# Kernel tuning notes

Hardware: AMD Instinct MI355X
Metric: run time of the kernel (lower is better)

Reference implementation:

```python
import jax, jax.numpy as jnp
import numpy as np

RANK = 16
ALPHA = 32.0
SCALING = ALPHA / RANK  # 2.0
IN_F = 2048
OUT_F = 2048


def setup_inputs() -> dict:
    key = jax.random.key(0)
    ks = jax.random.split(key, 6)
    bs, seq = 8, 2048
    n_splits, n_skills = 4, 8
    x = jax.random.normal(ks[0], (bs, seq, IN_F), dtype=jnp.float32)
    weights = jax.random.uniform(ks[1], (bs, n_splits, n_skills), dtype=jnp.float32)
    W = jax.random.normal(ks[2], (OUT_F, IN_F), dtype=jnp.float32) * 0.02
    bias = jax.random.normal(ks[3], (OUT_F,), dtype=jnp.float32) * 0.02
    lora_a = jax.random.normal(ks[4], (n_splits, n_skills, IN_F // n_splits, RANK), dtype=jnp.float32) * 0.02
    lora_b = jax.random.normal(ks[5], (n_splits, n_skills, RANK, OUT_F // n_splits), dtype=jnp.float32) * 0.02
    return {"x": x, "weights": weights, "W": W, "bias": bias, "lora_a": lora_a, "lora_b": lora_b}


def reference(x, weights, W, bias, lora_a, lora_b):
    bs = x.shape[0]
    # base linear layer
    layer_out = jnp.einsum('bti,oi->bto', x, W) + bias
    # skill-weighted mixing of per-split LoRA factors (soft routing)
    A = jnp.einsum('bqs,qsdr->bqdr', weights, lora_a)  # [bs, q, in/q, r]
    B = jnp.einsum('bqs,qsrd->bqrd', weights, lora_b)  # [bs, q, r, out/q]
    A = A.reshape(bs, IN_F, RANK)                      # [bs, in, r]
    B = jnp.transpose(B, (0, 2, 1, 3)).reshape(bs, RANK, OUT_F)  # [bs, r, out]
    # per-sample batched low-rank matmul + scaled residual add
    adapter = jnp.einsum('bti,bir->btr', x, A)
    adapter = jnp.einsum('btr,bro->bto', adapter, B) * SCALING
    return layer_out + adapter
```

## Files before the change

### kernel.cpp

```cpp
#include <hip/hip_runtime.h>


typedef __attribute__((ext_vector_type(8))) short short8;
typedef __attribute__((ext_vector_type(4))) float f32x4;

#define INF   2048
#define OUTF  2048
#define RANK  16
#define BM    128
#define BN    128
#define BK    32

__device__ __forceinline__ unsigned short bf16rne(float f) {
    unsigned int u = __float_as_uint(f);
    unsigned int r = u + 0x7FFFu + ((u >> 16) & 1u);
    return (unsigned short)(r >> 16);
}

__device__ __forceinline__ void gload_lds16(const void* g, void* l) {
    __builtin_amdgcn_global_load_lds(
        (const __attribute__((address_space(1))) unsigned int*)g,
        (__attribute__((address_space(3))) unsigned int*)l, 16, 0, 0);
}

__global__ __launch_bounds__(256) void k_wbf16(const float4* __restrict__ W,
                                               ushort4* __restrict__ o) {
    int g = blockIdx.x * 256 + threadIdx.x;
    float4 f = W[g];
    o[g] = make_ushort4(bf16rne(f.x), bf16rne(f.y), bf16rne(f.z), bf16rne(f.w));
}

__global__ __launch_bounds__(256) void k_mix(const float* __restrict__ wts,
                                             const float* __restrict__ la,
                                             const float* __restrict__ lb,
                                             float* __restrict__ Amix,
                                             float* __restrict__ Bmix) {
    int gid = blockIdx.x * 256 + threadIdx.x;
    int b = gid >> 11, i = gid & 2047;
    int q = i >> 9, d = i & 511;
    float w[8];
#pragma unroll
    for (int s = 0; s < 8; ++s) w[s] = wts[(b * 4 + q) * 8 + s];

    float accA[16];
#pragma unroll
    for (int r = 0; r < 16; ++r) accA[r] = 0.f;
#pragma unroll
    for (int s = 0; s < 8; ++s) {
        const float4* pa = (const float4*)(la + (((q * 8 + s) * 512 + d) << 4));
        float4 a0 = pa[0], a1 = pa[1], a2 = pa[2], a3 = pa[3];
        float wv = w[s];
        accA[0]  += wv * a0.x; accA[1]  += wv * a0.y; accA[2]  += wv * a0.z; accA[3]  += wv * a0.w;
        accA[4]  += wv * a1.x; accA[5]  += wv * a1.y; accA[6]  += wv * a1.z; accA[7]  += wv * a1.w;
        accA[8]  += wv * a2.x; accA[9]  += wv * a2.y; accA[10] += wv * a2.z; accA[11] += wv * a2.w;
        accA[12] += wv * a3.x; accA[13] += wv * a3.y; accA[14] += wv * a3.z; accA[15] += wv * a3.w;
    }
    float4* pA = (float4*)(Amix + ((size_t)gid << 4));
    pA[0] = make_float4(accA[0],  accA[1],  accA[2],  accA[3]);
    pA[1] = make_float4(accA[4],  accA[5],  accA[6],  accA[7]);
    pA[2] = make_float4(accA[8],  accA[9],  accA[10], accA[11]);
    pA[3] = make_float4(accA[12], accA[13], accA[14], accA[15]);

    float accB[16];
#pragma unroll
    for (int r = 0; r < 16; ++r) accB[r] = 0.f;
#pragma unroll
    for (int s = 0; s < 8; ++s) {
        float wv = w[s];
#pragma unroll
        for (int r = 0; r < 16; ++r)
            accB[r] += wv * lb[((q * 8 + s) * 16 + r) * 512 + d];
    }
#pragma unroll
    for (int r = 0; r < 16; ++r)
        Bmix[((size_t)(b * 16 + r) << 11) + i] = 2.0f * accB[r];
}

__global__ __launch_bounds__(256) void k_xa(const float* __restrict__ x,
                                            const float* __restrict__ Amix,
                                            float* __restrict__ T) {
    int row = blockIdx.x * 4 + (threadIdx.x >> 6);
    int lane = threadIdx.x & 63;
    int b = row >> 11;
    const float* xr = x + (size_t)row * INF;
    const float4* A4 = (const float4*)(Amix + ((size_t)b << 15));

    float acc[16];
#pragma unroll
    for (int r = 0; r < 16; ++r) acc[r] = 0.f;
    for (int k = lane; k < INF; k += 64) {
        float xv = xr[k];
        float4 a0 = A4[k * 4 + 0], a1 = A4[k * 4 + 1], a2 = A4[k * 4 + 2], a3 = A4[k * 4 + 3];
        acc[0]  += xv * a0.x; acc[1]  += xv * a0.y; acc[2]  += xv * a0.z; acc[3]  += xv * a0.w;
        acc[4]  += xv * a1.x; acc[5]  += xv * a1.y; acc[6]  += xv * a1.z; acc[7]  += xv * a1.w;
        acc[8]  += xv * a2.x; acc[9]  += xv * a2.y; acc[10] += xv * a2.z; acc[11] += xv * a2.w;
        acc[12] += xv * a3.x; acc[13] += xv * a3.y; acc[14] += xv * a3.z; acc[15] += xv * a3.w;
    }
#pragma unroll
    for (int off = 1; off < 64; off <<= 1) {
#pragma unroll
        for (int r = 0; r < 16; ++r) acc[r] += __shfl_xor(acc[r], off);
    }
    int r = lane & 15;
    float a0 = (r & 1) ? acc[1]  : acc[0];
    float a1 = (r & 1) ? acc[3]  : acc[2];
    float a2 = (r & 1) ? acc[5]  : acc[4];
    float a3 = (r & 1) ? acc[7]  : acc[6];
    float a4 = (r & 1) ? acc[9]  : acc[8];
    float a5 = (r & 1) ? acc[11] : acc[10];
    float a6 = (r & 1) ? acc[13] : acc[12];
    float a7 = (r & 1) ? acc[15] : acc[14];
    float b0 = (r & 2) ? a1 : a0;
    float b1 = (r & 2) ? a3 : a2;
    float b2 = (r & 2) ? a5 : a4;
    float b3 = (r & 2) ? a7 : a6;
    float c0 = (r & 4) ? b1 : b0;
    float c1 = (r & 4) ? b3 : b2;
    float v  = (r & 8) ? c1 : c0;
    if (lane < 16) T[((size_t)row << 4) + lane] = v;
}

__global__ __launch_bounds__(256)
void k_gemm(const float* __restrict__ x,
            const unsigned short* __restrict__ Wbf,
            const float* __restrict__ bias,
            const float* __restrict__ T,
            const float* __restrict__ Bmix,
            float* __restrict__ out) {
    __shared__ __align__(16) char smem[16384];
    unsigned short* ldsA = (unsigned short*)smem;
    unsigned short* ldsB = (unsigned short*)(smem + 8192);

    const int tid = threadIdx.x;
    const int wid = tid >> 6;
    const int lane = tid & 63;

    int swz = ((blockIdx.x & 7) << 8) | (blockIdx.x >> 3);
    const int m0 = (swz >> 4) << 7;
    const int n0 = (swz & 15) << 7;
    const int b  = m0 >> 11;

    const int wm = (wid >> 1) << 6;
    const int wn = (wid & 1) << 6;

    f32x4 acc[4][4];
#pragma unroll
    for (int i = 0; i < 4; ++i)
#pragma unroll
        for (int j = 0; j < 4; ++j) acc[i][j] = (f32x4){0.f, 0.f, 0.f, 0.f};

    const int ar = tid >> 3;
    const int ac = (tid & 7) << 2;
    const float* xbase = x + (size_t)(m0 + ar) * INF + ac;

    for (int kt = 0; kt < 64; ++kt) {
        const int k0 = kt << 5;
        __syncthreads();

#pragma unroll
        for (int c = 0; c < 2; ++c) {
            int rr = (wid << 5) + (c << 4);
            int srow = n0 + rr + (lane >> 2);
            int scol = k0 + ((lane & 3) << 3);
            gload_lds16(Wbf + (size_t)srow * INF + scol, &ldsB[rr * BK]);
        }
#pragma unroll
        for (int j = 0; j < 4; ++j) {
            float4 f = *(const float4*)(xbase + (size_t)(j * 32) * INF + k0);
            int rw = (ar + j * 32) * BK + ac;
            *(ushort4*)&ldsA[rw] =
                make_ushort4(bf16rne(f.x), bf16rne(f.y), bf16rne(f.z), bf16rne(f.w));
        }
        __syncthreads();

        short8 av[4], bv[4];
        const int fr = lane & 15;
        const int fs = (lane >> 4) << 3;
#pragma unroll
        for (int mf = 0; mf < 4; ++mf)
            av[mf] = *(const short8*)&ldsA[(wm + mf * 16 + fr) * BK + fs];
#pragma unroll
        for (int nf = 0; nf < 4; ++nf)
            bv[nf] = *(const short8*)&ldsB[(wn + nf * 16 + fr) * BK + fs];
#pragma unroll
        for (int mf = 0; mf < 4; ++mf)
#pragma unroll
            for (int nf = 0; nf < 4; ++nf)
                acc[mf][nf] = __builtin_amdgcn_mfma_f32_16x16x32_bf16(av[mf], bv[nf], acc[mf][nf], 0, 0, 0);
    }

    __syncthreads();
    float* ldsT  = (float*)smem;
    float* ldsB2 = (float*)(smem + 8192);
    {
        int row = tid >> 1, half = tid & 1;
        const float* Tp = T + (((size_t)(m0 + row)) << 4) + half * 8;
        float4 v0 = *(const float4*)Tp;
        float4 v1 = *(const float4*)(Tp + 4);
        int rb = half * 8;
        ldsT[(rb + 0) * 128 + row] = v0.x;
        ldsT[(rb + 1) * 128 + row] = v0.y;
        ldsT[(rb + 2) * 128 + row] = v0.z;
        ldsT[(rb + 3) * 128 + row] = v0.w;
        ldsT[(rb + 4) * 128 + row] = v1.x;
        ldsT[(rb + 5) * 128 + row] = v1.y;
        ldsT[(rb + 6) * 128 + row] = v1.z;
        ldsT[(rb + 7) * 128 + row] = v1.w;
        int r = tid >> 4, c8 = (tid & 15) << 3;
        const float* Bp = Bmix + ((size_t)(b * 16 + r) << 11) + n0 + c8;
        float4 u0 = *(const float4*)Bp;
        float4 u1 = *(const float4*)(Bp + 4);
        *(float4*)&ldsB2[r * 128 + c8]     = u0;
        *(float4*)&ldsB2[r * 128 + c8 + 4] = u1;
    }
    __syncthreads();

    const int fr = lane & 15;
    const int fq = lane >> 4;
#pragma unroll
    for (int r = 0; r < 16; ++r) {
        f32x4 tv[4];
#pragma unroll
        for (int mf = 0; mf < 4; ++mf)
            tv[mf] = *(const f32x4*)&ldsT[r * 128 + wm + mf * 16 + (fq << 2)];
        float bw[4];
#pragma unroll
        for (int nf = 0; nf < 4; ++nf)
            bw[nf] = ldsB2[r * 128 + wn + nf * 16 + fr];
#pragma unroll
        for (int mf = 0; mf < 4; ++mf)
#pragma unroll
            for (int nf = 0; nf < 4; ++nf)
                acc[mf][nf] += tv[mf] * bw[nf];
    }

#pragma unroll
    for (int nf = 0; nf < 4; ++nf) {
        int col = n0 + wn + nf * 16 + fr;
        float bv = bias[col];
#pragma unroll
        for (int mf = 0; mf < 4; ++mf) {
            int rbase = m0 + wm + mf * 16 + (fq << 2);
#pragma unroll
            for (int j = 0; j < 4; ++j)
                out[(size_t)(rbase + j) * OUTF + col] = acc[mf][nf][j] + bv;
        }
    }
}

extern "C" void kernel_launch(void* const* d_in, const int* in_sizes, int n_in,
                              void* d_out, int out_size, void* d_ws, size_t ws_size,
                              hipStream_t stream) {
    const float* x      = (const float*)d_in[0];
    const float* wts    = (const float*)d_in[1];
    const float* W      = (const float*)d_in[2];
    const float* bias   = (const float*)d_in[3];
    const float* lora_a = (const float*)d_in[4];
    const float* lora_b = (const float*)d_in[5];
    float* out = (float*)d_out;

    char* ws = (char*)d_ws;
    unsigned short* Wbf  = (unsigned short*)(ws);
    float*          Amix = (float*)(ws + (8u  << 20));
    float*          Bmix = (float*)(ws + (9u  << 20));
    float*          Tm   = (float*)(ws + (10u << 20));

    k_wbf16<<<4096, 256, 0, stream>>>((const float4*)W, (ushort4*)Wbf);
    k_mix  <<<64,   256, 0, stream>>>(wts, lora_a, lora_b, Amix, Bmix);
    k_xa   <<<4096, 256, 0, stream>>>(x, Amix, Tm);
    k_gemm <<<2048, 256, 0, stream>>>(x, Wbf, bias, Tm, Bmix, out);
}
```

Baseline: 611.0 us.

## Pre-convert x to bf16 in the x·A pass and stream both GEMM operands via LDS DMA

The x·A kernel now also writes a bf16 copy of x, so the main GEMM reads half the bytes per x tile and loads both operands with direct global-to-LDS loads instead of per-thread fp32 load, convert and store. The K tile grows from 32 to 64, with an XOR-swizzled LDS layout to avoid bank conflicts, which halves the number of barrier-separated iterations. The cost is an extra 64 MB bf16 write and read of x through the workspace and double the LDS per block, which may lower occupancy.

```diff
diff --git a/kernel.cpp b/kernel.cpp
--- a/kernel.cpp
+++ b/kernel.cpp
@@ -6,10 +6,9 @@
 
 #define INF   2048
 #define OUTF  2048
-#define RANK  16
 #define BM    128
 #define BN    128
-#define BK    32
+#define BK    64
 
 __device__ __forceinline__ unsigned short bf16rne(float f) {
     unsigned int u = __float_as_uint(f);
@@ -76,25 +75,37 @@
         Bmix[((size_t)(b * 16 + r) << 11) + i] = 2.0f * accB[r];
 }
 
-__global__ __launch_bounds__(256) void k_xa(const float* __restrict__ x,
-                                            const float* __restrict__ Amix,
-                                            float* __restrict__ T) {
+__global__ __launch_bounds__(256) void k_xsplit(const float4* __restrict__ x4,
+                                                const float* __restrict__ Amix,
+                                                ushort4* __restrict__ xbf,
+                                                float* __restrict__ T) {
     int row = blockIdx.x * 4 + (threadIdx.x >> 6);
     int lane = threadIdx.x & 63;
     int b = row >> 11;
-    const float* xr = x + (size_t)row * INF;
+    const float4* xr = x4 + (size_t)row * 512;
     const float4* A4 = (const float4*)(Amix + ((size_t)b << 15));
 
     float acc[16];
 #pragma unroll
     for (int r = 0; r < 16; ++r) acc[r] = 0.f;
-    for (int k = lane; k < INF; k += 64) {
-        float xv = xr[k];
-        float4 a0 = A4[k * 4 + 0], a1 = A4[k * 4 + 1], a2 = A4[k * 4 + 2], a3 = A4[k * 4 + 3];
-        acc[0]  += xv * a0.x; acc[1]  += xv * a0.y; acc[2]  += xv * a0.z; acc[3]  += xv * a0.w;
-        acc[4]  += xv * a1.x; acc[5]  += xv * a1.y; acc[6]  += xv * a1.z; acc[7]  += xv * a1.w;
-        acc[8]  += xv * a2.x; acc[9]  += xv * a2.y; acc[10] += xv * a2.z; acc[11] += xv * a2.w;
-        acc[12] += xv * a3.x; acc[13] += xv * a3.y; acc[14] += xv * a3.z; acc[15] += xv * a3.w;
+
+    for (int it = 0; it < 8; ++it) {
+        int f4 = lane + (it << 6);
+        float4 v = xr[f4];
+        xbf[(size_t)row * 512 + f4] =
+            make_ushort4(bf16rne(v.x), bf16rne(v.y), bf16rne(v.z), bf16rne(v.w));
+        int k0 = f4 << 2;
+        float xv[4] = {v.x, v.y, v.z, v.w};
+#pragma unroll
+        for (int j = 0; j < 4; ++j) {
+            const float4* ak = A4 + (size_t)(k0 + j) * 4;
+            float4 a0 = ak[0], a1 = ak[1], a2 = ak[2], a3 = ak[3];
+            float f = xv[j];
+            acc[0]  += f * a0.x; acc[1]  += f * a0.y; acc[2]  += f * a0.z; acc[3]  += f * a0.w;
+            acc[4]  += f * a1.x; acc[5]  += f * a1.y; acc[6]  += f * a1.z; acc[7]  += f * a1.w;
+            acc[8]  += f * a2.x; acc[9]  += f * a2.y; acc[10] += f * a2.z; acc[11] += f * a2.w;
+            acc[12] += f * a3.x; acc[13] += f * a3.y; acc[14] += f * a3.z; acc[15] += f * a3.w;
+        }
     }
 #pragma unroll
     for (int off = 1; off < 64; off <<= 1) {
@@ -121,15 +132,15 @@
 }
 
 __global__ __launch_bounds__(256)
-void k_gemm(const float* __restrict__ x,
+void k_gemm(const unsigned short* __restrict__ xbf,
             const unsigned short* __restrict__ Wbf,
             const float* __restrict__ bias,
             const float* __restrict__ T,
             const float* __restrict__ Bmix,
             float* __restrict__ out) {
-    __shared__ __align__(16) char smem[16384];
+    __shared__ __align__(16) char smem[32768];
     unsigned short* ldsA = (unsigned short*)smem;
-    unsigned short* ldsB = (unsigned short*)(smem + 8192);
+    unsigned short* ldsB = (unsigned short*)(smem + 16384);
 
     const int tid = threadIdx.x;
     const int wid = tid >> 6;
@@ -149,44 +160,45 @@
 #pragma unroll
         for (int j = 0; j < 4; ++j) acc[i][j] = (f32x4){0.f, 0.f, 0.f, 0.f};
 
-    const int ar = tid >> 3;
-    const int ac = (tid & 7) << 2;
-    const float* xbase = x + (size_t)(m0 + ar) * INF + ac;
-
-    for (int kt = 0; kt < 64; ++kt) {
-        const int k0 = kt << 5;
+    const int srow  = lane >> 3;
+    const int sslot = (lane & 7) ^ srow;
+    const unsigned short* xsrc = xbf + (size_t)(m0 + srow) * INF + (sslot << 3);
+    const unsigned short* wsrc = Wbf + (size_t)(n0 + srow) * INF + (sslot << 3);
+
+    for (int kt = 0; kt < 32; ++kt) {
+        const int k0 = kt << 6;
         __syncthreads();
-
-#pragma unroll
-        for (int c = 0; c < 2; ++c) {
-            int rr = (wid << 5) + (c << 4);
-            int srow = n0 + rr + (lane >> 2);
-            int scol = k0 + ((lane & 3) << 3);
-            gload_lds16(Wbf + (size_t)srow * INF + scol, &ldsB[rr * BK]);
-        }
-#pragma unroll
-        for (int j = 0; j < 4; ++j) {
-            float4 f = *(const float4*)(xbase + (size_t)(j * 32) * INF + k0);
-            int rw = (ar + j * 32) * BK + ac;
-            *(ushort4*)&ldsA[rw] =
-                make_ushort4(bf16rne(f.x), bf16rne(f.y), bf16rne(f.z), bf16rne(f.w));
+#pragma unroll
+        for (int c = 0; c < 4; ++c) {
+            int rr = (wid * 4 + c) << 3;
+            gload_lds16(xsrc + (size_t)rr * INF + k0, &ldsA[rr * BK]);
+            gload_lds16(wsrc + (size_t)rr * INF + k0, &ldsB[rr * BK]);
         }
         __syncthreads();
 
-        short8 av[4], bv[4];
         const int fr = lane & 15;
-        const int fs = (lane >> 4) << 3;
-#pragma unroll
-        for (int mf = 0; mf < 4; ++mf)
-            av[mf] = *(const short8*)&ldsA[(wm + mf * 16 + fr) * BK + fs];
-#pragma unroll
-        for (int nf = 0; nf < 4; ++nf)
-            bv[nf] = *(const short8*)&ldsB[(wn + nf * 16 + fr) * BK + fs];
-#pragma unroll
-        for (int mf = 0; mf < 4; ++mf)
-#pragma unroll
-            for (int nf = 0; nf < 4; ++nf)
-                acc[mf][nf] = __builtin_amdgcn_mfma_f32_16x16x32_bf16(av[mf], bv[nf], acc[mf][nf], 0, 0, 0);
+        const int sub = lane >> 4;
+#pragma unroll
+        for (int kk = 0; kk < 2; ++kk) {
+            short8 av[4], bv[4];
+#pragma unroll
+            for (int mf = 0; mf < 4; ++mf) {
+                int row = wm + mf * 16 + fr;
+                int sl = ((kk << 2) + sub) ^ (row & 7);
+                av[mf] = *(const short8*)&ldsA[(row << 6) + (sl << 3)];
+            }
+#pragma unroll
+            for (int nf = 0; nf < 4; ++nf) {
+                int row = wn + nf * 16 + fr;
+                int sl = ((kk << 2) + sub) ^ (row & 7);
+                bv[nf] = *(const short8*)&ldsB[(row << 6) + (sl << 3)];
+            }
+#pragma unroll
+            for (int mf = 0; mf < 4; ++mf)
+#pragma unroll
+                for (int nf = 0; nf < 4; ++nf)
+                    acc[mf][nf] = __builtin_amdgcn_mfma_f32_16x16x32_bf16(av[mf], bv[nf], acc[mf][nf], 0, 0, 0);
+        }
     }
 
     __syncthreads();
@@ -261,12 +273,13 @@
 
     char* ws = (char*)d_ws;
     unsigned short* Wbf  = (unsigned short*)(ws);
-    float*          Amix = (float*)(ws + (8u  << 20));
-    float*          Bmix = (float*)(ws + (9u  << 20));
-    float*          Tm   = (float*)(ws + (10u << 20));
-
-    k_wbf16<<<4096, 256, 0, stream>>>((const float4*)W, (ushort4*)Wbf);
-    k_mix  <<<64,   256, 0, stream>>>(wts, lora_a, lora_b, Amix, Bmix);
-    k_xa   <<<4096, 256, 0, stream>>>(x, Amix, Tm);
-    k_gemm <<<2048, 256, 0, stream>>>(x, Wbf, bias, Tm, Bmix, out);
-}
+    unsigned short* xbf  = (unsigned short*)(ws + (8u  << 20));
+    float*          Amix = (float*)(ws + (72u << 20));
+    float*          Bmix = (float*)(ws + (73u << 20));
+    float*          Tm   = (float*)(ws + (74u << 20));
+
+    k_wbf16 <<<4096, 256, 0, stream>>>((const float4*)W, (ushort4*)Wbf);
+    k_mix   <<<64,   256, 0, stream>>>(wts, lora_a, lora_b, Amix, Bmix);
+    k_xsplit<<<4096, 256, 0, stream>>>((const float4*)x, Amix, (ushort4*)xbf, Tm);
+    k_gemm  <<<2048, 256, 0, stream>>>(xbf, Wbf, bias, Tm, Bmix, out);
+}
```

Result: slower. 661.8 us (+8.3%).
